# Kernel tuning notes

Hardware: AMD Instinct MI355X
Metric: run time of the kernel (lower is better)

The kernel has to match this reference:

```python
import jax, jax.numpy as jnp
import numpy as np

N_NODES = 100000
N_EDGES = 1250000
D_FEAT = 64


def setup_inputs() -> dict:
    key = jax.random.key(0)
    k1, k2 = jax.random.split(key)
    x = jax.random.normal(k1, (N_NODES, D_FEAT), dtype=jnp.float32)
    edge_index = jax.random.randint(k2, (2, N_EDGES), 0, N_NODES, dtype=jnp.int64)
    return {"t": 0, "x": x, "edge_index": edge_index}


def reference(t, x, edge_index):
    # LGConv(normalize=False): out[i] = sum_{(j->i) in E} x[j]
    # adj_t SpMM expressed as gather + segment-sum scatter.
    src = edge_index[0]  # source/neighbor nodes
    dst = edge_index[1]  # destination nodes
    msgs = x[src]  # [E, D] gather
    out = jax.ops.segment_sum(msgs, dst, num_segments=N_NODES)  # [N, D]
    return out
```

## Files before the change

### kernel.cpp

```cpp
#include <hip/hip_runtime.h>

#define N_NODES 100000
#define N_EDGES 1250000
#define D_FEAT 64

#define NB_SHIFT 7
#define NODES_PER_B 128
#define N_BUCKETS ((N_NODES + NODES_PER_B - 1) / NODES_PER_B)
#define TROW (N_BUCKETS + 1)
#define NB_PAD 1024
#define MAX_BUCKET_EDGES 2048
#define SRC_BITS 17
#define SRC_MASK ((1u << SRC_BITS) - 1u)

#define CH 8192
#define NCH ((N_EDGES + CH - 1) / CH)

__global__ __launch_bounds__(256) void lgconv_scatter(
    const float* __restrict__ x, const int* __restrict__ src,
    const int* __restrict__ dst, float* __restrict__ out) {
    int tid  = blockIdx.x * blockDim.x + threadIdx.x;
    int edge = tid >> 4;
    int f4   = (tid & 15) << 2;
    if (edge >= N_EDGES) return;
    int s = src[edge], d = dst[edge];
    const float4 v = *reinterpret_cast<const float4*>(x + (size_t)s * D_FEAT + f4);
    float* o = out + (size_t)d * D_FEAT + f4;
    unsafeAtomicAdd(o + 0, v.x); unsafeAtomicAdd(o + 1, v.y);
    unsafeAtomicAdd(o + 2, v.z); unsafeAtomicAdd(o + 3, v.w);
}

__device__ __forceinline__ unsigned short f2bf(float f) {
    unsigned int u = __float_as_uint(f);
    return (unsigned short)((u + 0x7FFFu + ((u >> 16) & 1u)) >> 16);
}
__device__ __forceinline__ float bflo(unsigned int p) {
    return __uint_as_float(p << 16);
}
__device__ __forceinline__ float bfhi(unsigned int p) {
    return __uint_as_float(p & 0xFFFF0000u);
}

template <bool CONV>
__global__ __launch_bounds__(1024) void k1_sort(
    const float* __restrict__ x, unsigned short* __restrict__ xb,
    const int* __restrict__ src, const int* __restrict__ dst,
    unsigned int* __restrict__ bins, int* __restrict__ table) {
    __shared__ int hist[NB_PAD];
    __shared__ int scanBase[NB_PAD];
    __shared__ int cur[NB_PAD];
    __shared__ int scanTmp[1024];
    __shared__ unsigned int stage[CH];
    const int t    = threadIdx.x;
    const int c    = blockIdx.x;
    const int base = c * CH;
    const int cnt  = min(CH, N_EDGES - base);

    if (CONV) {
        const int F4 = N_NODES * D_FEAT / 4;
        for (int i = c * 1024 + t; i < F4; i += NCH * 1024) {
            float4 v = reinterpret_cast<const float4*>(x)[i];
            ushort4 o;
            o.x = f2bf(v.x); o.y = f2bf(v.y); o.z = f2bf(v.z); o.w = f2bf(v.w);
            reinterpret_cast<ushort4*>(xb)[i] = o;
        }
    }

    hist[t] = 0; cur[t] = 0;
    __syncthreads();
    for (int i = t; i < cnt; i += 1024)
        atomicAdd(&hist[dst[base + i] >> NB_SHIFT], 1);
    __syncthreads();
    int v = hist[t];
    scanTmp[t] = v;
    __syncthreads();
    for (int off = 1; off < 1024; off <<= 1) {
        int u = (t >= off) ? scanTmp[t - off] : 0;
        __syncthreads();
        scanTmp[t] += u;
        __syncthreads();
    }
    scanBase[t] = scanTmp[t] - v;
    __syncthreads();
    if (t < TROW) table[c * TROW + t] = scanBase[t];
    for (int i = t; i < cnt; i += 1024) {
        int d = dst[base + i], s = src[base + i];
        int b = d >> NB_SHIFT;
        unsigned int packed = ((unsigned int)(d & (NODES_PER_B - 1)) << SRC_BITS)
                            | (unsigned int)s;
        int pos = scanBase[b] + atomicAdd(&cur[b], 1);
        stage[pos] = packed;
    }
    __syncthreads();
    for (int i = t; i < cnt; i += 1024) bins[base + i] = stage[i];
}

template <bool BF>
__global__ __launch_bounds__(512) void k2_accum(
    const float* __restrict__ x, const unsigned short* __restrict__ xb,
    const unsigned int* __restrict__ bins, const int* __restrict__ table,
    float* __restrict__ out) {
    __shared__ int            startA[512];
    __shared__ unsigned short lenA[512];
    __shared__ int            destB[512];
    __shared__ int            scanTmp[512];
    __shared__ unsigned int   raw[MAX_BUCKET_EDGES];
    __shared__ unsigned int   srcs[MAX_BUCKET_EDGES];
    __shared__ int cntArr[NODES_PER_B];
    __shared__ int nodeOff[NODES_PER_B + 1];
    __shared__ int curN[NODES_PER_B];
    __shared__ int s2[NODES_PER_B];
    const int t = threadIdx.x;
    const int b = blockIdx.x;

    int st = 0, len = 0;
    if (t < NCH) {
        st  = table[t * TROW + b];
        len = table[t * TROW + b + 1] - st;
    }
    startA[t] = st;
    lenA[t]   = (unsigned short)len;
    scanTmp[t] = len;
    __syncthreads();
    for (int off = 1; off < 512; off <<= 1) {
        int u = (t >= off) ? scanTmp[t - off] : 0;
        __syncthreads();
        scanTmp[t] += u;
        __syncthreads();
    }
    destB[t] = scanTmp[t] - len;
    int cntTot = scanTmp[511];
    if (cntTot > MAX_BUCKET_EDGES) cntTot = MAX_BUCKET_EDGES;
    if (t < NODES_PER_B) cntArr[t] = 0;
    __syncthreads();

    {
        const int cj = t >> 4;
        const int jj = t & 15;
        for (int c0 = 0; c0 < NCH; c0 += 32) {
            int c = c0 + cj;
            if (c < NCH) {
                int l = lenA[c], s0 = startA[c], db = destB[c];
                const unsigned int* p = bins + (size_t)c * CH + s0;
                if (jj < l) raw[db + jj] = p[jj];
                if (jj == 15)
                    for (int q = 16; q < l; ++q) raw[db + q] = p[q];
            }
        }
    }
    __syncthreads();

    for (int i = t; i < cntTot; i += 512)
        atomicAdd(&cntArr[raw[i] >> SRC_BITS], 1);
    __syncthreads();
    int v = (t < NODES_PER_B) ? cntArr[t] : 0;
    if (t < NODES_PER_B) s2[t] = v;
    __syncthreads();
    for (int off = 1; off < NODES_PER_B; off <<= 1) {
        int u = (t < NODES_PER_B && t >= off) ? s2[t - off] : 0;
        __syncthreads();
        if (t < NODES_PER_B) s2[t] += u;
        __syncthreads();
    }
    if (t < NODES_PER_B) { nodeOff[t] = s2[t] - v; curN[t] = s2[t] - v; }
    if (t == 0) nodeOff[NODES_PER_B] = cntTot;
    __syncthreads();
    for (int i = t; i < cntTot; i += 512) {
        unsigned int p = raw[i];
        int pos = atomicAdd(&curN[p >> SRC_BITS], 1);
        srcs[pos] = p & SRC_MASK;
    }
    __syncthreads();

    if (BF) {
        int f0 = (t & 7) << 3;
        for (int g = 0; g < NODES_PER_B / 64; ++g) {
            int local = g * 64 + (t >> 3);
            int node  = b * NODES_PER_B + local;
            int beg = nodeOff[local], end = nodeOff[local + 1];
            float a0=0,a1=0,a2=0,a3=0,a4=0,a5=0,a6=0,a7=0;
            int k = beg;
            for (; k + 3 < end; k += 4) {
                const uint4 u0 = *reinterpret_cast<const uint4*>(
                    xb + (size_t)srcs[k] * D_FEAT + f0);
                const uint4 u1 = *reinterpret_cast<const uint4*>(
                    xb + (size_t)srcs[k + 1] * D_FEAT + f0);
                const uint4 u2 = *reinterpret_cast<const uint4*>(
                    xb + (size_t)srcs[k + 2] * D_FEAT + f0);
                const uint4 u3 = *reinterpret_cast<const uint4*>(
                    xb + (size_t)srcs[k + 3] * D_FEAT + f0);
                a0 += bflo(u0.x) + bflo(u1.x) + bflo(u2.x) + bflo(u3.x);
                a1 += bfhi(u0.x) + bfhi(u1.x) + bfhi(u2.x) + bfhi(u3.x);
                a2 += bflo(u0.y) + bflo(u1.y) + bflo(u2.y) + bflo(u3.y);
                a3 += bfhi(u0.y) + bfhi(u1.y) + bfhi(u2.y) + bfhi(u3.y);
                a4 += bflo(u0.z) + bflo(u1.z) + bflo(u2.z) + bflo(u3.z);
                a5 += bfhi(u0.z) + bfhi(u1.z) + bfhi(u2.z) + bfhi(u3.z);
                a6 += bflo(u0.w) + bflo(u1.w) + bflo(u2.w) + bflo(u3.w);
                a7 += bfhi(u0.w) + bfhi(u1.w) + bfhi(u2.w) + bfhi(u3.w);
            }
            for (; k < end; ++k) {
                const uint4 u = *reinterpret_cast<const uint4*>(
                    xb + (size_t)srcs[k] * D_FEAT + f0);
                a0 += bflo(u.x); a1 += bfhi(u.x);
                a2 += bflo(u.y); a3 += bfhi(u.y);
                a4 += bflo(u.z); a5 += bfhi(u.z);
                a6 += bflo(u.w); a7 += bfhi(u.w);
            }
            if (node < N_NODES) {
                float* op = out + (size_t)node * D_FEAT + f0;
                *reinterpret_cast<float4*>(op)     = make_float4(a0, a1, a2, a3);
                *reinterpret_cast<float4*>(op + 4) = make_float4(a4, a5, a6, a7);
            }
        }
    } else {
        int lane4 = (t & 15) << 2;
        for (int g = 0; g < NODES_PER_B / 32; ++g) {
            int local = g * 32 + (t >> 4);
            int node  = b * NODES_PER_B + local;
            int beg = nodeOff[local], end = nodeOff[local + 1];
            float4 acc = make_float4(0.f, 0.f, 0.f, 0.f);
            int k = beg;
            for (; k + 1 < end; k += 2) {
                unsigned int i0 = srcs[k], i1 = srcs[k + 1];
                const float4 a = *reinterpret_cast<const float4*>(x + (size_t)i0 * D_FEAT + lane4);
                const float4 c = *reinterpret_cast<const float4*>(x + (size_t)i1 * D_FEAT + lane4);
                acc.x += a.x + c.x; acc.y += a.y + c.y;
                acc.z += a.z + c.z; acc.w += a.w + c.w;
            }
            if (k < end) {
                unsigned int i0 = srcs[k];
                const float4 a = *reinterpret_cast<const float4*>(x + (size_t)i0 * D_FEAT + lane4);
                acc.x += a.x; acc.y += a.y; acc.z += a.z; acc.w += a.w;
            }
            if (node < N_NODES)
                *reinterpret_cast<float4*>(out + (size_t)node * D_FEAT + lane4) = acc;
        }
    }
}

extern "C" void kernel_launch(void* const* d_in, const int* in_sizes, int n_in,
                              void* d_out, int out_size, void* d_ws, size_t ws_size,
                              hipStream_t stream) {
    const float* x   = (const float*)d_in[1];
    const int*   ei  = (const int*)d_in[2];
    const int*   src = ei;
    const int*   dst = ei + N_EDGES;
    float*       out = (float*)d_out;

    const size_t tabBytes = (size_t)NCH * TROW * sizeof(int);
    const size_t binBytes = (size_t)N_EDGES * sizeof(unsigned int);
    const size_t xbOff    = (binBytes + tabBytes + 15) & ~(size_t)15;
    const size_t needA    = xbOff + (size_t)N_NODES * D_FEAT * sizeof(unsigned short);
    const size_t needB    = binBytes + tabBytes;

    if (ws_size >= needA) {
        unsigned int*   bins  = (unsigned int*)d_ws;
        int*            table = (int*)((char*)d_ws + binBytes);
        unsigned short* xb    = (unsigned short*)((char*)d_ws + xbOff);
        k1_sort<true><<<NCH, 1024, 0, stream>>>(x, xb, src, dst, bins, table);
        k2_accum<true><<<N_BUCKETS, 512, 0, stream>>>(x, xb, bins, table, out);
    } else if (ws_size >= needB) {
        unsigned int* bins  = (unsigned int*)d_ws;
        int*          table = (int*)((char*)d_ws + binBytes);
        k1_sort<false><<<NCH, 1024, 0, stream>>>(x, nullptr, src, dst, bins, table);
        k2_accum<false><<<N_BUCKETS, 512, 0, stream>>>(x, nullptr, bins, table, out);
    } else {
        hipMemsetAsync(out, 0, (size_t)out_size * sizeof(float), stream);
        const int total = N_EDGES * 16;
        lgconv_scatter<<<(total + 255) / 256, 256, 0, stream>>>(x, src, dst, out);
    }
}
```

Before: 138.2 us.

## Use wavefront shuffle scans, transposed ushort chunk table, and smaller sort chunks

Replaces the shared-memory Hillis-Steele block scans in both kernels with wavefront shuffle scans, which removes many __syncthreads barriers. The chunk offset table becomes a transposed unsigned-short array, so the accumulate kernel reads it with coalesced loads. Chunk size drops from 8192 to 4992, giving about 251 sort blocks to spread across CUs, and the gather loop uses 8 lanes per chunk with a strided copy. The cost is more chunks and segments for each bucket to gather. A segment of 8 lanes may also underuse bandwidth when a bucket's per-chunk segments are long.

After: 134.5 us. 1.03x faster.

```diff
diff --git a/kernel.cpp b/kernel.cpp
--- a/kernel.cpp
+++ b/kernel.cpp
@@ -13,8 +13,9 @@
 #define SRC_BITS 17
 #define SRC_MASK ((1u << SRC_BITS) - 1u)
 
-#define CH 8192
+#define CH 4992
 #define NCH ((N_EDGES + CH - 1) / CH)
+#define NCHP 256
 
 __global__ __launch_bounds__(256) void lgconv_scatter(
     const float* __restrict__ x, const int* __restrict__ src,
@@ -41,20 +42,32 @@
     return __uint_as_float(p & 0xFFFF0000u);
 }
 
+__device__ __forceinline__ int wscan_incl(int v) {
+    const int lane = threadIdx.x & 63;
+#pragma unroll
+    for (int off = 1; off < 64; off <<= 1) {
+        int u = __shfl_up(v, off, 64);
+        if (lane >= off) v += u;
+    }
+    return v;
+}
+
 template <bool CONV>
 __global__ __launch_bounds__(1024) void k1_sort(
     const float* __restrict__ x, unsigned short* __restrict__ xb,
     const int* __restrict__ src, const int* __restrict__ dst,
-    unsigned int* __restrict__ bins, int* __restrict__ table) {
+    unsigned int* __restrict__ bins, unsigned short* __restrict__ tableT) {
     __shared__ int hist[NB_PAD];
     __shared__ int scanBase[NB_PAD];
     __shared__ int cur[NB_PAD];
-    __shared__ int scanTmp[1024];
+    __shared__ int wsum[16];
     __shared__ unsigned int stage[CH];
     const int t    = threadIdx.x;
     const int c    = blockIdx.x;
     const int base = c * CH;
     const int cnt  = min(CH, N_EDGES - base);
+    const int lane = t & 63;
+    const int wid  = t >> 6;
 
     if (CONV) {
         const int F4 = N_NODES * D_FEAT / 4;
@@ -71,23 +84,28 @@
     for (int i = t; i < cnt; i += 1024)
         atomicAdd(&hist[dst[base + i] >> NB_SHIFT], 1);
     __syncthreads();
+
     int v = hist[t];
-    scanTmp[t] = v;
-    __syncthreads();
-    for (int off = 1; off < 1024; off <<= 1) {
-        int u = (t >= off) ? scanTmp[t - off] : 0;
-        __syncthreads();
-        scanTmp[t] += u;
-        __syncthreads();
-    }
-    scanBase[t] = scanTmp[t] - v;
-    __syncthreads();
-    if (t < TROW) table[c * TROW + t] = scanBase[t];
+    int s = wscan_incl(v);
+    if (lane == 63) wsum[wid] = s;
+    __syncthreads();
+    if (t < 16) {
+        int w  = wsum[t];
+        int ws = wscan_incl(w);
+        wsum[t] = ws;
+    }
+    __syncthreads();
+    int incl = s + (wid ? wsum[wid - 1] : 0);
+    scanBase[t] = incl - v;
+    __syncthreads();
+
+    if (t < TROW) tableT[(size_t)t * NCHP + c] = (unsigned short)scanBase[t];
+
     for (int i = t; i < cnt; i += 1024) {
-        int d = dst[base + i], s = src[base + i];
+        int d = dst[base + i], sv = src[base + i];
         int b = d >> NB_SHIFT;
         unsigned int packed = ((unsigned int)(d & (NODES_PER_B - 1)) << SRC_BITS)
-                            | (unsigned int)s;
+                            | (unsigned int)sv;
         int pos = scanBase[b] + atomicAdd(&cur[b], 1);
         stage[pos] = packed;
     }
@@ -98,53 +116,54 @@
 template <bool BF>
 __global__ __launch_bounds__(512) void k2_accum(
     const float* __restrict__ x, const unsigned short* __restrict__ xb,
-    const unsigned int* __restrict__ bins, const int* __restrict__ table,
+    const unsigned int* __restrict__ bins, const unsigned short* __restrict__ tableT,
     float* __restrict__ out) {
     __shared__ int            startA[512];
     __shared__ unsigned short lenA[512];
     __shared__ int            destB[512];
-    __shared__ int            scanTmp[512];
     __shared__ unsigned int   raw[MAX_BUCKET_EDGES];
     __shared__ unsigned int   srcs[MAX_BUCKET_EDGES];
     __shared__ int cntArr[NODES_PER_B];
     __shared__ int nodeOff[NODES_PER_B + 1];
     __shared__ int curN[NODES_PER_B];
-    __shared__ int s2[NODES_PER_B];
-    const int t = threadIdx.x;
-    const int b = blockIdx.x;
+    __shared__ int wsum[8];
+    const int t    = threadIdx.x;
+    const int b    = blockIdx.x;
+    const int lane = t & 63;
+    const int wid  = t >> 6;
 
     int st = 0, len = 0;
     if (t < NCH) {
-        st  = table[t * TROW + b];
-        len = table[t * TROW + b + 1] - st;
+        st  = tableT[(size_t)b * NCHP + t];
+        len = (int)tableT[(size_t)(b + 1) * NCHP + t] - st;
     }
     startA[t] = st;
     lenA[t]   = (unsigned short)len;
-    scanTmp[t] = len;
-    __syncthreads();
-    for (int off = 1; off < 512; off <<= 1) {
-        int u = (t >= off) ? scanTmp[t - off] : 0;
-        __syncthreads();
-        scanTmp[t] += u;
-        __syncthreads();
-    }
-    destB[t] = scanTmp[t] - len;
-    int cntTot = scanTmp[511];
+    if (t < NODES_PER_B) cntArr[t] = 0;
+    int s = wscan_incl(len);
+    if (lane == 63) wsum[wid] = s;
+    __syncthreads();
+    if (t < 8) {
+        int w  = wsum[t];
+        int ws = wscan_incl(w);
+        wsum[t] = ws;
+    }
+    __syncthreads();
+    int incl = s + (wid ? wsum[wid - 1] : 0);
+    destB[t] = incl - len;
+    int cntTot = wsum[7];
     if (cntTot > MAX_BUCKET_EDGES) cntTot = MAX_BUCKET_EDGES;
-    if (t < NODES_PER_B) cntArr[t] = 0;
     __syncthreads();
 
     {
-        const int cj = t >> 4;
-        const int jj = t & 15;
-        for (int c0 = 0; c0 < NCH; c0 += 32) {
+        const int cj = t >> 3;
+        const int jj = t & 7;
+        for (int c0 = 0; c0 < NCH; c0 += 64) {
             int c = c0 + cj;
             if (c < NCH) {
                 int l = lenA[c], s0 = startA[c], db = destB[c];
                 const unsigned int* p = bins + (size_t)c * CH + s0;
-                if (jj < l) raw[db + jj] = p[jj];
-                if (jj == 15)
-                    for (int q = 16; q < l; ++q) raw[db + q] = p[q];
+                for (int q = jj; q < l; q += 8) raw[db + q] = p[q];
             }
         }
     }
@@ -153,16 +172,15 @@
     for (int i = t; i < cntTot; i += 512)
         atomicAdd(&cntArr[raw[i] >> SRC_BITS], 1);
     __syncthreads();
-    int v = (t < NODES_PER_B) ? cntArr[t] : 0;
-    if (t < NODES_PER_B) s2[t] = v;
-    __syncthreads();
-    for (int off = 1; off < NODES_PER_B; off <<= 1) {
-        int u = (t < NODES_PER_B && t >= off) ? s2[t - off] : 0;
-        __syncthreads();
-        if (t < NODES_PER_B) s2[t] += u;
-        __syncthreads();
-    }
-    if (t < NODES_PER_B) { nodeOff[t] = s2[t] - v; curN[t] = s2[t] - v; }
+    int v2 = (t < NODES_PER_B) ? cntArr[t] : 0;
+    int s2 = wscan_incl(v2);
+    if (t < NODES_PER_B && lane == 63) wsum[wid] = s2;
+    __syncthreads();
+    if (t < NODES_PER_B) {
+        int excl = s2 + ((wid == 1) ? wsum[0] : 0) - v2;
+        nodeOff[t] = excl;
+        curN[t]    = excl;
+    }
     if (t == 0) nodeOff[NODES_PER_B] = cntTot;
     __syncthreads();
     for (int i = t; i < cntTot; i += 512) {
@@ -247,23 +265,23 @@
     const int*   dst = ei + N_EDGES;
     float*       out = (float*)d_out;
 
-    const size_t tabBytes = (size_t)NCH * TROW * sizeof(int);
+    const size_t tabBytes = (size_t)TROW * NCHP * sizeof(unsigned short);
     const size_t binBytes = (size_t)N_EDGES * sizeof(unsigned int);
     const size_t xbOff    = (binBytes + tabBytes + 15) & ~(size_t)15;
     const size_t needA    = xbOff + (size_t)N_NODES * D_FEAT * sizeof(unsigned short);
     const size_t needB    = binBytes + tabBytes;
 
     if (ws_size >= needA) {
-        unsigned int*   bins  = (unsigned int*)d_ws;
-        int*            table = (int*)((char*)d_ws + binBytes);
-        unsigned short* xb    = (unsigned short*)((char*)d_ws + xbOff);
-        k1_sort<true><<<NCH, 1024, 0, stream>>>(x, xb, src, dst, bins, table);
-        k2_accum<true><<<N_BUCKETS, 512, 0, stream>>>(x, xb, bins, table, out);
+        unsigned int*   bins   = (unsigned int*)d_ws;
+        unsigned short* tableT = (unsigned short*)((char*)d_ws + binBytes);
+        unsigned short* xb     = (unsigned short*)((char*)d_ws + xbOff);
+        k1_sort<true><<<NCH, 1024, 0, stream>>>(x, xb, src, dst, bins, tableT);
+        k2_accum<true><<<N_BUCKETS, 512, 0, stream>>>(x, xb, bins, tableT, out);
     } else if (ws_size >= needB) {
-        unsigned int* bins  = (unsigned int*)d_ws;
-        int*          table = (int*)((char*)d_ws + binBytes);
-        k1_sort<false><<<NCH, 1024, 0, stream>>>(x, nullptr, src, dst, bins, table);
-        k2_accum<false><<<N_BUCKETS, 512, 0, stream>>>(x, nullptr, bins, table, out);
+        unsigned int*   bins   = (unsigned int*)d_ws;
+        unsigned short* tableT = (unsigned short*)((char*)d_ws + binBytes);
+        k1_sort<false><<<NCH, 1024, 0, stream>>>(x, nullptr, src, dst, bins, tableT);
+        k2_accum<false><<<N_BUCKETS, 512, 0, stream>>>(x, nullptr, bins, tableT, out);
     } else {
         hipMemsetAsync(out, 0, (size_t)out_size * sizeof(float), stream);
         const int total = N_EDGES * 16;
```
